# Kernel tuning notes

Measured on AMD Instinct MI355X. Metric: run time of the kernel, lower is better.

Reference implementation:

```python
import jax, jax.numpy as jnp
import numpy as np

N_HEAD = 12

def setup_inputs() -> dict:
    key = jax.random.key(0)
    ks = jax.random.split(key, 5)
    C = 768
    B, T = 2, 2048
    s = 0.02
    x = jax.random.normal(ks[0], (B, T, C), dtype=jnp.float32)
    W_attn = jax.random.normal(ks[1], (C, 3 * C), dtype=jnp.float32) * s
    b_attn = jnp.zeros((3 * C,), dtype=jnp.float32)
    W_proj = jax.random.normal(ks[2], (C, C), dtype=jnp.float32) * s
    b_proj = jnp.zeros((C,), dtype=jnp.float32)
    return {"x": x, "W_attn": W_attn, "b_attn": b_attn, "W_proj": W_proj, "b_proj": b_proj}

def reference(x, W_attn, b_attn, W_proj, b_proj):
    B, T, C = x.shape
    H = N_HEAD
    hs = C // H
    qkv = x @ W_attn + b_attn                      # [B,T,3C]
    q, k, v = jnp.split(qkv, 3, axis=2)
    # [B,H,T,hs]
    q = q.reshape(B, T, H, hs).transpose(0, 2, 1, 3)
    k = k.reshape(B, T, H, hs).transpose(0, 2, 1, 3)
    v = v.reshape(B, T, H, hs).transpose(0, 2, 1, 3)
    scale = 1.0 / np.sqrt(hs).astype(np.float32)
    att = jnp.einsum('bhqd,bhkd->bhqk', q, k) * scale   # [B,H,T,T]
    causal = jnp.tril(jnp.ones((T, T), dtype=bool))
    att = jnp.where(causal, att, -jnp.inf)
    att = jax.nn.softmax(att, axis=-1)
    y = jnp.einsum('bhqk,bhkd->bhqd', att, v)            # [B,H,T,hs]
    y = y.transpose(0, 2, 1, 3).reshape(B, T, C)
    return y @ W_proj + b_proj
```

## Files before the change

### kernel.cpp

```cpp
#include <hip/hip_runtime.h>


#define BB 2
#define TT 2048
#define CC 768
#define C3 2304
#define HH 12
#define DD 64
#define MM 4096

typedef unsigned short u16;
typedef unsigned int u32;
typedef __attribute__((ext_vector_type(8))) u16 u16x8;
typedef __attribute__((ext_vector_type(8))) __bf16 bf16x8;
typedef __attribute__((ext_vector_type(4))) float f32x4;

__device__ __forceinline__ float u2f(u16 u) {
    union { u32 i; float f; } c; c.i = ((u32)u) << 16; return c.f;
}
__device__ __forceinline__ u16 f2u(float f) {
    union { float f; u32 i; } c; c.f = f;
    u32 x = c.i;
    return (u16)((x + 0x7FFFu + ((x >> 16) & 1u)) >> 16);
}
__device__ __forceinline__ u16 f2b(float f) {
    __bf16 h = (__bf16)f; return __builtin_bit_cast(u16, h);
}
__device__ __forceinline__ bf16x8 ldsb8(const u16* p) {
    return __builtin_bit_cast(bf16x8, *(const u16x8*)p);
}
__device__ __forceinline__ f32x4 mfma16(bf16x8 a, bf16x8 b, f32x4 c) {
    return __builtin_amdgcn_mfma_f32_16x16x32_bf16(a, b, c, 0, 0, 0);
}
typedef __attribute__((address_space(1))) const u32 gu32;
typedef __attribute__((address_space(3))) u32 lu32;
__device__ __forceinline__ void gload16(const u16* gp, u16* lp) {
    __builtin_amdgcn_global_load_lds((gu32*)(const void*)gp, (lu32*)(void*)lp,
                                     16, 0, 0);
}
__device__ __forceinline__ void barrier_raw() {
    asm volatile("" ::: "memory");
    __builtin_amdgcn_s_barrier();
    asm volatile("" ::: "memory");
}

__global__ void detect_kernel(const u16* __restrict__ x, int* __restrict__ flag)
{
    __shared__ int found;
    if (threadIdx.x == 0) found = 0;
    __syncthreads();
    int local = 0;
    const u16x8* p = (const u16x8*)x + threadIdx.x;
    #pragma unroll
    for (int i = 0; i < 8; ++i) {
        const u16x8 v = p[(size_t)i * 256];
        #pragma unroll
        for (int j = 0; j < 8; ++j)
            if ((v[j] & 0x7F80u) == 0x7F80u) local = 1;
    }
    if (local) atomicOr(&found, 1);
    __syncthreads();
    if (threadIdx.x == 0) *flag = found ? 1 : 0;
}

__device__ void prep_w_body(const void* __restrict__ Wv, u16* __restrict__ Wt,
                            int K, int N, int bx, int by, int fm,
                            u16 (*Ts)[72])
{
    const int t = threadIdx.x;
    const int n0 = bx * 64, k0 = by * 64;
    const int r = t >> 2, c0 = (t & 3) << 4;

    if (fm) {
        const float* W = (const float*)Wv + (size_t)(k0 + r) * N + n0 + c0;
        #pragma unroll
        for (int i = 0; i < 16; i += 4) {
            const float4 v = *(const float4*)(W + i);
            Ts[c0 + i + 0][r] = f2u(v.x);
            Ts[c0 + i + 1][r] = f2u(v.y);
            Ts[c0 + i + 2][r] = f2u(v.z);
            Ts[c0 + i + 3][r] = f2u(v.w);
        }
    } else {
        const u16* W = (const u16*)Wv + (size_t)(k0 + r) * N + n0 + c0;
        const u16x8 a = *(const u16x8*)W;
        const u16x8 c = *(const u16x8*)(W + 8);
        #pragma unroll
        for (int i = 0; i < 8; ++i) { Ts[c0 + i][r] = a[i]; Ts[c0 + 8 + i][r] = c[i]; }
    }
    __syncthreads();
    u16* o = Wt + (size_t)(n0 + r) * K + k0 + c0;
    *(u16x8*)o = *(const u16x8*)&Ts[r][c0];
    *(u16x8*)(o + 8) = *(const u16x8*)&Ts[r][c0 + 8];
}

__global__ __launch_bounds__(256)
void fused_prep(const void* __restrict__ x, const void* __restrict__ Wa,
                const void* __restrict__ ba, const void* __restrict__ Wp,
                const void* __restrict__ bp,
                u16* __restrict__ xb, u16* __restrict__ WaT,
                u16* __restrict__ WpT, u16* __restrict__ bao,
                u16* __restrict__ bpo,
                const int* __restrict__ flag, int mode)
{
    __shared__ u16 Ts[64][72];
    const int fm = (mode >= 0) ? mode : *flag;
    const int blk = blockIdx.x;
    const int t = threadIdx.x;

    if (blk < 432) {
        prep_w_body(Wa, WaT, CC, C3, blk % 36, blk / 36, fm, Ts);
    } else if (blk < 576) {
        const int b2 = blk - 432;
        prep_w_body(Wp, WpT, CC, CC, b2 % 12, b2 / 12, fm, Ts);
    } else if (blk < 2112) {
        const size_t i = (size_t)(blk - 576) * 256 + t;
        if (fm) {
            const float* xp = (const float*)x + i * 8;
            u16x8 o;
            #pragma unroll
            for (int j = 0; j < 8; ++j) o[j] = f2u(xp[j]);
            *(u16x8*)(xb + i * 8) = o;
        } else {
            *(u16x8*)(xb + i * 8) = *(const u16x8*)((const u16*)x + i * 8);
        }
    } else {
        const int i = (blk - 2112) * 256 + t;
        if (i < C3) bao[i] = fm ? f2u(((const float*)ba)[i]) : ((const u16*)ba)[i];
        if (i < CC) bpo[i] = fm ? f2u(((const float*)bp)[i]) : ((const u16*)bp)[i];
    }
}

template <int FR>
__global__ __launch_bounds__(256)
void gemm_mfma(const u16* __restrict__ A, const u16* __restrict__ Bt,
               const u16* __restrict__ bias, void* __restrict__ outv,
               int M, int N, int K, const int* __restrict__ flag,
               int mode, int om_sel)
{
    constexpr int TS = 32 * FR;
    constexpr int LPW = FR / 2;

    __shared__ u16 As[2][TS * 32];
    __shared__ u16 Bs[2][TS * 32];

    const int t = threadIdx.x;
    const int lane = t & 63, wave = t >> 6;
    const int wm = wave >> 1, wn = wave & 1;
    const int l15 = lane & 15, h4 = lane >> 4;
    const int m0 = blockIdx.y * TS, n0 = blockIdx.x * TS;
    const int om = om_sel ? ((mode >= 0) ? mode : *flag) : 0;

    const int rowA = wave * (TS / 4) + (lane >> 2);
    const int cs = ((lane & 3) ^ ((lane >> 4) & 3)) * 8;
    const u16* Ab[LPW];
    const u16* Bb[LPW];
    #pragma unroll
    for (int j = 0; j < LPW; ++j) {
        Ab[j] = A + (size_t)(m0 + rowA + 16 * j) * K + cs;
        Bb[j] = Bt + (size_t)(n0 + rowA + 16 * j) * K + cs;
    }
    const int dst = wave * LPW * 512;

    f32x4 acc[FR][FR];
    #pragma unroll
    for (int i = 0; i < FR; ++i)
        #pragma unroll
        for (int j = 0; j < FR; ++j) acc[i][j] = (f32x4){0.f, 0.f, 0.f, 0.f};

    const int csr = (h4 ^ (l15 >> 2)) * 8;
    const int arow = wm * (TS / 2) + l15;
    const int brow = wn * (TS / 2) + l15;

    const int NT = K >> 5;
    #pragma unroll
    for (int j = 0; j < LPW; ++j) {
        gload16(Ab[j], &As[0][dst + j * 512]);
        gload16(Bb[j], &Bs[0][dst + j * 512]);
    }

    for (int kt = 0; kt < NT; ++kt) {
        const int cur = kt & 1;
        if (kt + 1 < NT) {
            const int k0 = (kt + 1) << 5;
            const int nb = cur ^ 1;
            #pragma unroll
            for (int j = 0; j < LPW; ++j) {
                gload16(Ab[j] + k0, &As[nb][dst + j * 512]);
                gload16(Bb[j] + k0, &Bs[nb][dst + j * 512]);
            }
            if constexpr (FR == 4)
                asm volatile("s_waitcnt vmcnt(4)" ::: "memory");
            else
                asm volatile("s_waitcnt vmcnt(2)" ::: "memory");
        } else {
            asm volatile("s_waitcnt vmcnt(0)" ::: "memory");
        }
        barrier_raw();

        bf16x8 af[FR], bfr[FR];
        #pragma unroll
        for (int f = 0; f < FR; ++f) {
            af[f]  = ldsb8(&As[cur][(arow + f * 16) * 32 + csr]);
            bfr[f] = ldsb8(&Bs[cur][(brow + f * 16) * 32 + csr]);
        }
        #pragma unroll
        for (int i = 0; i < FR; ++i)
            #pragma unroll
            for (int j = 0; j < FR; ++j)
                acc[i][j] = mfma16(af[i], bfr[j], acc[i][j]);

        barrier_raw();
    }

    const int orow = m0 + wm * (TS / 2) + h4 * 4;
    const int ocol = n0 + wn * (TS / 2) + l15;
    if (om == 0) {
        u16* out = (u16*)outv;
        #pragma unroll
        for (int i = 0; i < FR; ++i)
            #pragma unroll
            for (int j = 0; j < FR; ++j) {
                const int col = ocol + j * 16;
                const float bv = u2f(bias[col]);
                #pragma unroll
                for (int r2 = 0; r2 < 4; ++r2)
                    out[(size_t)(orow + i * 16 + r2) * N + col] = f2b(acc[i][j][r2] + bv);
            }
    } else {
        float* out = (float*)outv;
        #pragma unroll
        for (int i = 0; i < FR; ++i)
            #pragma unroll
            for (int j = 0; j < FR; ++j) {
                const int col = ocol + j * 16;
                const float bv = u2f(bias[col]);
                #pragma unroll
                for (int r2 = 0; r2 < 4; ++r2)
                    out[(size_t)(orow + i * 16 + r2) * N + col] = acc[i][j][r2] + bv;
            }
    }
}

__global__ __launch_bounds__(256)
void attn_mfma(const u16* __restrict__ qkv, u16* __restrict__ yatt)
{
    __shared__ u16 Ks[2][64][72];
    __shared__ u16 Vt[2][64][72];

    const int bid = blockIdx.x;
    const int bin = bid & 255, slot = bid >> 8;
    const int g = bin >> 5, j = bin & 31;
    int qt;
    if (slot == 0)      qt = j;
    else if (slot == 1) qt = (j + 16) & 31;
    else                qt = (j < 16) ? (30 - 2 * j) : (63 - 2 * j);
    const int hb = slot * 8 + g;
    const int h = hb % HH, b = hb / HH;

    const int t = threadIdx.x;
    const int lane = t & 63, w = t >> 6;
    const int l15 = lane & 15, h4 = lane >> 4;
    const int q0 = qt * 64;

    const int sr = t >> 2;
    const int sd = (t & 3) << 4;
    const int rho = ((sr >> 5) & 1) * 32 + ((sr >> 2) & 1) * 16 +
                    ((sr >> 3) & 3) * 4 + (sr & 3);
    const int vk = (t & 31) * 2;
    const int vd = (t >> 5) << 3;

    bf16x8 aq0, aq1;
    {
        const u16* qp = qkv + ((size_t)(b * TT + q0 + w * 16 + l15)) * C3
                        + h * DD + h4 * 8;
        const u16x8 v0 = *(const u16x8*)qp;
        const u16x8 v1 = *(const u16x8*)(qp + 32);
        #pragma unroll
        for (int i = 0; i < 8; ++i) {
            aq0[i] = (__bf16)(u2f(v0[i]) * 0.125f);
            aq1[i] = (__bf16)(u2f(v1[i]) * 0.125f);
        }
    }

    float m_i = -1e30f, l_i = 0.f;
    f32x4 O[4];
    #pragma unroll
    for (int d = 0; d < 4; ++d) O[d] = (f32x4){0.f, 0.f, 0.f, 0.f};

    const u16* kB = qkv + ((size_t)(b * TT + sr)) * C3 + CC + h * DD + sd;
    const u16* vB = qkv + ((size_t)(b * TT + vk)) * C3 + 2 * CC + h * DD + vd;

    const int NT = qt + 1;

    u16x8 kr0 = *(const u16x8*)kB;
    u16x8 kr1 = *(const u16x8*)(kB + 8);
    u16x8 vr0 = *(const u16x8*)vB;
    u16x8 vr1 = *(const u16x8*)(vB + C3);
    *(u16x8*)&Ks[0][rho][sd]     = kr0;
    *(u16x8*)&Ks[0][rho][sd + 8] = kr1;
    #pragma unroll
    for (int i = 0; i < 8; ++i)
        *(u32*)&Vt[0][vd + i][vk] = (u32)vr0[i] | ((u32)vr1[i] << 16);
    if (NT > 1) {
        const u16* kp = kB + (size_t)64 * C3;
        const u16* vp = vB + (size_t)64 * C3;
        kr0 = *(const u16x8*)kp;
        kr1 = *(const u16x8*)(kp + 8);
        vr0 = *(const u16x8*)vp;
        vr1 = *(const u16x8*)(vp + C3);
    }
    __syncthreads();

    const int qg = q0 + w * 16 + l15;

    for (int kt = 0; kt < NT; ++kt) {
        const int cur = kt & 1;

        f32x4 s[4];
        __builtin_amdgcn_s_setprio(1);
        #pragma unroll
        for (int kf = 0; kf < 4; ++kf) {
            f32x4 z = (f32x4){0.f, 0.f, 0.f, 0.f};
            z = mfma16(ldsb8(&Ks[cur][kf * 16 + l15][h4 * 8]), aq0, z);
            z = mfma16(ldsb8(&Ks[cur][kf * 16 + l15][32 + h4 * 8]), aq1, z);
            s[kf] = z;
        }
        __builtin_amdgcn_s_setprio(0);

        if (kt + 1 < NT) {
            const int nb = cur ^ 1;
            *(u16x8*)&Ks[nb][rho][sd]     = kr0;
            *(u16x8*)&Ks[nb][rho][sd + 8] = kr1;
            #pragma unroll
            for (int i = 0; i < 8; ++i)
                *(u32*)&Vt[nb][vd + i][vk] = (u32)vr0[i] | ((u32)vr1[i] << 16);
            if (kt + 2 < NT) {
                const u16* kp = kB + (size_t)(kt + 2) * 64 * C3;
                const u16* vp = vB + (size_t)(kt + 2) * 64 * C3;
                kr0 = *(const u16x8*)kp;
                kr1 = *(const u16x8*)(kp + 8);
                vr0 = *(const u16x8*)vp;
                vr1 = *(const u16x8*)(vp + C3);
            }
        }

        if (kt == qt) {
            #pragma unroll
            for (int kf = 0; kf < 4; ++kf) {
                const int kbase = kt * 64 + 8 * h4 + 32 * (kf >> 1) + 4 * (kf & 1);
                #pragma unroll
                for (int r2 = 0; r2 < 4; ++r2)
                    if (kbase + r2 > qg) s[kf][r2] = -1e30f;
            }
        }

        float mx = s[0][0];
        #pragma unroll
        for (int kf = 0; kf < 4; ++kf)
            #pragma unroll
            for (int r2 = 0; r2 < 4; ++r2) mx = fmaxf(mx, s[kf][r2]);
        mx = fmaxf(mx, __shfl_xor(mx, 16));
        mx = fmaxf(mx, __shfl_xor(mx, 32));
        const float mnew = fmaxf(m_i, mx);
        const float a_ = __expf(m_i - mnew);

        bf16x8 ap, ap2;
        float rs = 0.f;
        #pragma unroll
        for (int kf = 0; kf < 2; ++kf)
            #pragma unroll
            for (int r2 = 0; r2 < 4; ++r2) {
                const float p = __expf(s[kf][r2] - mnew);
                rs += p;
                ap[kf * 4 + r2] = (__bf16)p;
            }
        #pragma unroll
        for (int kf = 2; kf < 4; ++kf)
            #pragma unroll
            for (int r2 = 0; r2 < 4; ++r2) {
                const float p = __expf(s[kf][r2] - mnew);
                rs += p;
                ap2[(kf - 2) * 4 + r2] = (__bf16)p;
            }
        rs += __shfl_xor(rs, 16);
        rs += __shfl_xor(rs, 32);
        l_i = l_i * a_ + rs;
        m_i = mnew;

        float alf[4];
        #pragma unroll
        for (int r2 = 0; r2 < 4; ++r2) alf[r2] = __shfl(a_, h4 * 4 + r2);
        #pragma unroll
        for (int d = 0; d < 4; ++d)
            #pragma unroll
            for (int r2 = 0; r2 < 4; ++r2) O[d][r2] *= alf[r2];

        __builtin_amdgcn_s_setprio(1);
        #pragma unroll
        for (int d = 0; d < 4; ++d) {
            O[d] = mfma16(ap,  ldsb8(&Vt[cur][d * 16 + l15][h4 * 8]), O[d]);
            O[d] = mfma16(ap2, ldsb8(&Vt[cur][d * 16 + l15][32 + h4 * 8]), O[d]);
        }
        __builtin_amdgcn_s_setprio(0);

        __syncthreads();
    }

    const float invl = 1.0f / l_i;
    float inv[4];
    #pragma unroll
    for (int r2 = 0; r2 < 4; ++r2) inv[r2] = __shfl(invl, h4 * 4 + r2);
    u16* yp = yatt + ((size_t)(b * TT + q0 + w * 16 + h4 * 4)) * CC + h * DD + l15;
    #pragma unroll
    for (int r2 = 0; r2 < 4; ++r2)
        #pragma unroll
        for (int d = 0; d < 4; ++d)
            yp[(size_t)r2 * CC + d * 16] = f2b(O[d][r2] * inv[r2]);
}

extern "C" void kernel_launch(void* const* d_in, const int* in_sizes, int n_in,
                              void* d_out, int out_size, void* d_ws, size_t ws_size,
                              hipStream_t stream)
{
    (void)n_in; (void)out_size; (void)ws_size;

    const void* x      = d_in[0];
    const void* W_attn = d_in[1];
    const void* b_attn = d_in[2];
    const void* W_proj = d_in[3];
    const void* b_proj = d_in[4];

    u16* qkv  = (u16*)d_ws;
    u16* yatt = qkv + (size_t)MM * C3;
    u16* xb   = yatt;
    u16* WaT  = yatt + (size_t)MM * CC;
    u16* WpT  = WaT + (size_t)C3 * CC;
    u16* ba   = WpT + (size_t)CC * CC;
    u16* bp   = ba + C3;
    int* flag = (int*)(bp + CC);

    int mode = -1;
    if (in_sizes[0] == MM * CC * 4) mode = 1;
    else if (in_sizes[0] == MM * CC * 2) mode = 0;
    if (mode < 0) {
        detect_kernel<<<1, 256, 0, stream>>>((const u16*)x, flag);
    }

    fused_prep<<<2121, 256, 0, stream>>>(x, W_attn, b_attn, W_proj, b_proj,
                                         xb, WaT, WpT, ba, bp, flag, mode);

    gemm_mfma<4><<<dim3(C3 / 128, MM / 128), 256, 0, stream>>>(
        xb, WaT, ba, (void*)qkv, MM, C3, CC, flag, mode, 0);

    attn_mfma<<<dim3(TT / 64 * HH * BB, 1, 1), 256, 0, stream>>>(qkv, yatt);

    gemm_mfma<2><<<dim3(CC / 64, MM / 64), 256, 0, stream>>>(
        yatt, WpT, bp, d_out, MM, CC, CC, flag, mode, 1);
}
```

Before: 170.6 us.

## Use rectangular GEMM tiles with XCD-aware block remap and lazy softmax rescaling

The GEMM is generalized to separate M/N fragment counts, so the QKV projection uses 128x64 tiles for more blocks. Block indices are remapped with a stride-8 swizzle so that neighbouring tiles land on the same XCD. When the input is already bf16, the prep kernel skips the x copy and the GEMM reads x directly. The attention kernel now rescales the running max and output only when some row's new max exceeds the old one by more than 8. It also keeps per-lane partial row sums and reduces them across lanes once at the end, which removes per-tile shuffles at some risk of exp overflow headroom.

New measurement: 162.9 us. 1.05x faster.

```diff
diff --git a/kernel.cpp b/kernel.cpp
--- a/kernel.cpp
+++ b/kernel.cpp
@@ -114,16 +114,13 @@
         const int b2 = blk - 432;
         prep_w_body(Wp, WpT, CC, CC, b2 % 12, b2 / 12, fm, Ts);
     } else if (blk < 2112) {
+        if (fm == 0) return;
         const size_t i = (size_t)(blk - 576) * 256 + t;
-        if (fm) {
-            const float* xp = (const float*)x + i * 8;
-            u16x8 o;
-            #pragma unroll
-            for (int j = 0; j < 8; ++j) o[j] = f2u(xp[j]);
-            *(u16x8*)(xb + i * 8) = o;
-        } else {
-            *(u16x8*)(xb + i * 8) = *(const u16x8*)((const u16*)x + i * 8);
-        }
+        const float* xp = (const float*)x + i * 8;
+        u16x8 o;
+        #pragma unroll
+        for (int j = 0; j < 8; ++j) o[j] = f2u(xp[j]);
+        *(u16x8*)(xb + i * 8) = o;
     } else {
         const int i = (blk - 2112) * 256 + t;
         if (i < C3) bao[i] = fm ? f2u(((const float*)ba)[i]) : ((const u16*)ba)[i];
@@ -131,53 +128,62 @@
     }
 }
 
-template <int FR>
+template <int FRM, int FRN>
 __global__ __launch_bounds__(256)
-void gemm_mfma(const u16* __restrict__ A, const u16* __restrict__ Bt,
-               const u16* __restrict__ bias, void* __restrict__ outv,
-               int M, int N, int K, const int* __restrict__ flag,
-               int mode, int om_sel)
-{
-    constexpr int TS = 32 * FR;
-    constexpr int LPW = FR / 2;
-
-    __shared__ u16 As[2][TS * 32];
-    __shared__ u16 Bs[2][TS * 32];
+void gemm_mfma(const u16* __restrict__ Adir, const u16* __restrict__ Acnv,
+               const u16* __restrict__ Bt, const u16* __restrict__ bias,
+               void* __restrict__ outv, int M, int N, int K,
+               const int* __restrict__ flag, int mode, int om_sel)
+{
+    constexpr int TSM = 32 * FRM, TSN = 32 * FRN;
+    constexpr int LPA = TSM / 64;
+    constexpr int LPB = TSN / 64;
+
+    __shared__ u16 As[2][TSM * 32];
+    __shared__ u16 Bs[2][TSN * 32];
+
+    const int fm = (mode >= 0) ? mode : *flag;
+    const u16* A = fm ? Acnv : Adir;
+    const int om = om_sel ? fm : 0;
+
+    const int nwg = gridDim.x;
+    const int lin = (blockIdx.x & 7) * (nwg >> 3) + (blockIdx.x >> 3);
+    const int nx = N / TSN;
+    const int m0 = (lin / nx) * TSM, n0 = (lin % nx) * TSN;
 
     const int t = threadIdx.x;
     const int lane = t & 63, wave = t >> 6;
     const int wm = wave >> 1, wn = wave & 1;
     const int l15 = lane & 15, h4 = lane >> 4;
-    const int m0 = blockIdx.y * TS, n0 = blockIdx.x * TS;
-    const int om = om_sel ? ((mode >= 0) ? mode : *flag) : 0;
-
-    const int rowA = wave * (TS / 4) + (lane >> 2);
+
+    const int rsub = lane >> 2;
     const int cs = ((lane & 3) ^ ((lane >> 4) & 3)) * 8;
-    const u16* Ab[LPW];
-    const u16* Bb[LPW];
-    #pragma unroll
-    for (int j = 0; j < LPW; ++j) {
-        Ab[j] = A + (size_t)(m0 + rowA + 16 * j) * K + cs;
-        Bb[j] = Bt + (size_t)(n0 + rowA + 16 * j) * K + cs;
-    }
-    const int dst = wave * LPW * 512;
-
-    f32x4 acc[FR][FR];
-    #pragma unroll
-    for (int i = 0; i < FR; ++i)
-        #pragma unroll
-        for (int j = 0; j < FR; ++j) acc[i][j] = (f32x4){0.f, 0.f, 0.f, 0.f};
+    const u16* Ab[LPA];
+    const u16* Bb[LPB];
+    #pragma unroll
+    for (int j = 0; j < LPA; ++j)
+        Ab[j] = A + (size_t)(m0 + wave * (16 * LPA) + j * 16 + rsub) * K + cs;
+    #pragma unroll
+    for (int j = 0; j < LPB; ++j)
+        Bb[j] = Bt + (size_t)(n0 + wave * (16 * LPB) + j * 16 + rsub) * K + cs;
+
+    f32x4 acc[FRM][FRN];
+    #pragma unroll
+    for (int i = 0; i < FRM; ++i)
+        #pragma unroll
+        for (int j = 0; j < FRN; ++j) acc[i][j] = (f32x4){0.f, 0.f, 0.f, 0.f};
 
     const int csr = (h4 ^ (l15 >> 2)) * 8;
-    const int arow = wm * (TS / 2) + l15;
-    const int brow = wn * (TS / 2) + l15;
+    const int arow = wm * (TSM / 2) + l15;
+    const int brow = wn * (TSN / 2) + l15;
 
     const int NT = K >> 5;
     #pragma unroll
-    for (int j = 0; j < LPW; ++j) {
-        gload16(Ab[j], &As[0][dst + j * 512]);
-        gload16(Bb[j], &Bs[0][dst + j * 512]);
-    }
+    for (int j = 0; j < LPA; ++j)
+        gload16(Ab[j], &As[0][(wave * LPA + j) * 512]);
+    #pragma unroll
+    for (int j = 0; j < LPB; ++j)
+        gload16(Bb[j], &Bs[0][(wave * LPB + j) * 512]);
 
     for (int kt = 0; kt < NT; ++kt) {
         const int cur = kt & 1;
@@ -185,12 +191,15 @@
             const int k0 = (kt + 1) << 5;
             const int nb = cur ^ 1;
             #pragma unroll
-            for (int j = 0; j < LPW; ++j) {
-                gload16(Ab[j] + k0, &As[nb][dst + j * 512]);
-                gload16(Bb[j] + k0, &Bs[nb][dst + j * 512]);
-            }
-            if constexpr (FR == 4)
+            for (int j = 0; j < LPA; ++j)
+                gload16(Ab[j] + k0, &As[nb][(wave * LPA + j) * 512]);
+            #pragma unroll
+            for (int j = 0; j < LPB; ++j)
+                gload16(Bb[j] + k0, &Bs[nb][(wave * LPB + j) * 512]);
+            if constexpr (LPA + LPB == 4)
                 asm volatile("s_waitcnt vmcnt(4)" ::: "memory");
+            else if constexpr (LPA + LPB == 3)
+                asm volatile("s_waitcnt vmcnt(3)" ::: "memory");
             else
                 asm volatile("s_waitcnt vmcnt(2)" ::: "memory");
         } else {
@@ -198,29 +207,30 @@
         }
         barrier_raw();
 
-        bf16x8 af[FR], bfr[FR];
-        #pragma unroll
-        for (int f = 0; f < FR; ++f) {
-            af[f]  = ldsb8(&As[cur][(arow + f * 16) * 32 + csr]);
+        bf16x8 af[FRM], bfr[FRN];
+        #pragma unroll
+        for (int f = 0; f < FRM; ++f)
+            af[f] = ldsb8(&As[cur][(arow + f * 16) * 32 + csr]);
+        #pragma unroll
+        for (int f = 0; f < FRN; ++f)
             bfr[f] = ldsb8(&Bs[cur][(brow + f * 16) * 32 + csr]);
-        }
-        #pragma unroll
-        for (int i = 0; i < FR; ++i)
-            #pragma unroll
-            for (int j = 0; j < FR; ++j)
+        #pragma unroll
+        for (int i = 0; i < FRM; ++i)
+            #pragma unroll
+            for (int j = 0; j < FRN; ++j)
                 acc[i][j] = mfma16(af[i], bfr[j], acc[i][j]);
 
         barrier_raw();
     }
 
-    const int orow = m0 + wm * (TS / 2) + h4 * 4;
-    const int ocol = n0 + wn * (TS / 2) + l15;
+    const int orow = m0 + wm * (TSM / 2) + h4 * 4;
+    const int ocol = n0 + wn * (TSN / 2) + l15;
     if (om == 0) {
         u16* out = (u16*)outv;
         #pragma unroll
-        for (int i = 0; i < FR; ++i)
-            #pragma unroll
-            for (int j = 0; j < FR; ++j) {
+        for (int i = 0; i < FRM; ++i)
+            #pragma unroll
+            for (int j = 0; j < FRN; ++j) {
                 const int col = ocol + j * 16;
                 const float bv = u2f(bias[col]);
                 #pragma unroll
@@ -230,9 +240,9 @@
     } else {
         float* out = (float*)outv;
         #pragma unroll
-        for (int i = 0; i < FR; ++i)
-            #pragma unroll
-            for (int j = 0; j < FR; ++j) {
+        for (int i = 0; i < FRM; ++i)
+            #pragma unroll
+            for (int j = 0; j < FRN; ++j) {
                 const int col = ocol + j * 16;
                 const float bv = u2f(bias[col]);
                 #pragma unroll
@@ -283,7 +293,7 @@
         }
     }
 
-    float m_i = -1e30f, l_i = 0.f;
+    float m_i = -1e30f, l_p = 0.f;
     f32x4 O[4];
     #pragma unroll
     for (int d = 0; d < 4; ++d) O[d] = (f32x4){0.f, 0.f, 0.f, 0.f};
@@ -355,15 +365,28 @@
             }
         }
 
-        float mx = s[0][0];
+        float pm = s[0][0];
         #pragma unroll
         for (int kf = 0; kf < 4; ++kf)
             #pragma unroll
-            for (int r2 = 0; r2 < 4; ++r2) mx = fmaxf(mx, s[kf][r2]);
-        mx = fmaxf(mx, __shfl_xor(mx, 16));
-        mx = fmaxf(mx, __shfl_xor(mx, 32));
-        const float mnew = fmaxf(m_i, mx);
-        const float a_ = __expf(m_i - mnew);
+            for (int r2 = 0; r2 < 4; ++r2) pm = fmaxf(pm, s[kf][r2]);
+
+        if (!__all(pm <= m_i + 8.f)) {
+            float pr = pm;
+            pr = fmaxf(pr, __shfl_xor(pr, 16));
+            pr = fmaxf(pr, __shfl_xor(pr, 32));
+            const float mnew = fmaxf(m_i, pr);
+            const float a_ = __expf(m_i - mnew);
+            l_p *= a_;
+            float alf[4];
+            #pragma unroll
+            for (int r2 = 0; r2 < 4; ++r2) alf[r2] = __shfl(a_, h4 * 4 + r2);
+            #pragma unroll
+            for (int d = 0; d < 4; ++d)
+                #pragma unroll
+                for (int r2 = 0; r2 < 4; ++r2) O[d][r2] *= alf[r2];
+            m_i = mnew;
+        }
 
         bf16x8 ap, ap2;
         float rs = 0.f;
@@ -371,7 +394,7 @@
         for (int kf = 0; kf < 2; ++kf)
             #pragma unroll
             for (int r2 = 0; r2 < 4; ++r2) {
-                const float p = __expf(s[kf][r2] - mnew);
+                const float p = __expf(s[kf][r2] - m_i);
                 rs += p;
                 ap[kf * 4 + r2] = (__bf16)p;
             }
@@ -379,22 +402,11 @@
         for (int kf = 2; kf < 4; ++kf)
             #pragma unroll
             for (int r2 = 0; r2 < 4; ++r2) {
-                const float p = __expf(s[kf][r2] - mnew);
+                const float p = __expf(s[kf][r2] - m_i);
                 rs += p;
                 ap2[(kf - 2) * 4 + r2] = (__bf16)p;
             }
-        rs += __shfl_xor(rs, 16);
-        rs += __shfl_xor(rs, 32);
-        l_i = l_i * a_ + rs;
-        m_i = mnew;
-
-        float alf[4];
-        #pragma unroll
-        for (int r2 = 0; r2 < 4; ++r2) alf[r2] = __shfl(a_, h4 * 4 + r2);
-        #pragma unroll
-        for (int d = 0; d < 4; ++d)
-            #pragma unroll
-            for (int r2 = 0; r2 < 4; ++r2) O[d][r2] *= alf[r2];
+        l_p += rs;
 
         __builtin_amdgcn_s_setprio(1);
         #pragma unroll
@@ -407,7 +419,10 @@
         __syncthreads();
     }
 
-    const float invl = 1.0f / l_i;
+    float lr = l_p;
+    lr += __shfl_xor(lr, 16);
+    lr += __shfl_xor(lr, 32);
+    const float invl = 1.0f / lr;
     float inv[4];
     #pragma unroll
     for (int r2 = 0; r2 < 4; ++r2) inv[r2] = __shfl(invl, h4 * 4 + r2);
@@ -450,11 +465,11 @@
     fused_prep<<<2121, 256, 0, stream>>>(x, W_attn, b_attn, W_proj, b_proj,
                                          xb, WaT, WpT, ba, bp, flag, mode);
 
-    gemm_mfma<4><<<dim3(C3 / 128, MM / 128), 256, 0, stream>>>(
-        xb, WaT, ba, (void*)qkv, MM, C3, CC, flag, mode, 0);
+    gemm_mfma<4, 2><<<(MM / 128) * (C3 / 64), 256, 0, stream>>>(
+        (const u16*)x, xb, WaT, ba, (void*)qkv, MM, C3, CC, flag, mode, 0);
 
     attn_mfma<<<dim3(TT / 64 * HH * BB, 1, 1), 256, 0, stream>>>(qkv, yatt);
 
-    gemm_mfma<2><<<dim3(CC / 64, MM / 64), 256, 0, stream>>>(
-        yatt, WpT, bp, d_out, MM, CC, CC, flag, mode, 1);
-}
+    gemm_mfma<2, 2><<<(MM / 64) * (CC / 64), 256, 0, stream>>>(
+        yatt, yatt, WpT, bp, d_out, MM, CC, CC, flag, mode, 1);
+}
```
